# Optimization experiments

Measured on AMD Instinct MI355X. Metric: run time of the kernel, lower is better.

The kernel has to match this reference:

```python
import jax, jax.numpy as jnp
import numpy as np

Bsz, T, N, Dm = 4, 256, 32, 128
L, S, DC = 2, 16, 4          # num_layers, d_state, d_conv
DI = 2 * Dm                   # d_inner (expand=2)
DTR = Dm // 16                # dt_rank = ceil(128/16) = 8
K, R = 4, 16                  # K_bases, rank
MAX_DT = 0.2

def _silu(x):
    return x * jax.nn.sigmoid(x)

def _causal_dwconv(x, w, b):
    # x: [BN, T, DI], w: [DI, DC] depthwise, left-pad DC-1 (== pad DC-1 both sides then [:T])
    xc = jnp.swapaxes(x, 1, 2)  # [BN, DI, T]
    y = jax.lax.conv_general_dilated(xc, w[:, None, :], (1,), [(DC - 1, 0)],
                                     feature_group_count=DI,
                                     dimension_numbers=('NCH', 'OIH', 'NCH'))
    return jnp.swapaxes(y + b[None, :, None], 1, 2)

def _selective_scan(x, dt, Bm, Cm, A):
    # x, dt: [BN,T,DI]; Bm, Cm: [BN,T,S]; A: [DI,S]
    def step(carry, inp):
        dt_t, B_t, C_t, x_t = inp
        dA = jnp.exp(dt_t[:, :, None] * A)                      # [BN,DI,S]
        carry = dA * carry + dt_t[:, :, None] * B_t[:, None, :] * x_t[:, :, None]
        y = jnp.einsum('bds,bs->bd', carry, C_t)
        return carry, y
    BN = x.shape[0]
    carry0 = jnp.zeros((BN, DI, S), x.dtype)
    seq = (jnp.swapaxes(dt, 0, 1), jnp.swapaxes(Bm, 0, 1),
           jnp.swapaxes(Cm, 0, 1), jnp.swapaxes(x, 0, 1))
    _, ys = jax.lax.scan(step, carry0, seq)
    return jnp.swapaxes(ys, 0, 1)

def _mamba(h, in_w, cw, cb, xw, dtw, dtb, A_log, Dp, ow):
    xz = h @ in_w.T                          # [BN,T,2*DI]
    xh, z = xz[..., :DI], xz[..., DI:]
    xh = _silu(_causal_dwconv(xh, cw, cb))
    x_dbl = xh @ xw.T                        # [BN,T,DTR+2S]
    dt = jax.nn.softplus(x_dbl[..., :DTR] @ dtw.T + dtb)
    Bm = x_dbl[..., DTR:DTR + S]
    Cm = x_dbl[..., DTR + S:]
    A = -jnp.exp(A_log)
    y = _selective_scan(xh, dt, Bm, Cm, A) + Dp * xh
    return (y * _silu(z)) @ ow.T

def setup_inputs():
    ks = jax.random.split(jax.random.key(0), 32)
    n = lambda i, shp, s: jax.random.normal(ks[i], shp, jnp.float32) * s
    sD = 1.0 / np.sqrt(Dm); sI = 1.0 / np.sqrt(DI)
    return {
        'x': n(0, (Bsz, T, N, Dm), 1.0),
        'in_proj_w': n(1, (L, 2 * DI, Dm), sD),
        'conv_w': n(2, (L, DI, DC), 1.0 / np.sqrt(DC)),
        'conv_b': n(3, (L, DI), 0.01),
        'x_proj_w': n(4, (L, DTR + 2 * S, DI), sI),
        'dt_proj_w': n(5, (L, DI, DTR), 1.0 / np.sqrt(DTR)),
        'dt_proj_b': jnp.full((L, DI), -4.0, jnp.float32) + n(6, (L, DI), 0.1),
        'A_log': jnp.tile(jnp.log(jnp.arange(1, S + 1, dtype=jnp.float32))[None, None, :], (L, DI, 1)),
        'D_skip': jnp.ones((L, DI), jnp.float32),
        'out_proj_w': n(7, (L, Dm, DI), sI),
        'U': n(8, (K, Dm, R), sD),
        'V': n(9, (K, R, Dm), sD),
        'A_scale': jnp.full((K,), 0.3, jnp.float32),
        'gate_w1': n(10, (Dm, Dm), sD), 'gate_b1': jnp.zeros((Dm,), jnp.float32),
        'gate_w2': n(11, (K + 1, Dm), sD), 'gate_b2': jnp.zeros((K + 1,), jnp.float32),
        'film_g_w': n(12, (Dm, Dm), sD), 'film_g_b': jnp.zeros((Dm,), jnp.float32),
        'film_b_w': n(13, (Dm, Dm), sD), 'film_b_b': jnp.zeros((Dm,), jnp.float32),
        'mix_w1': n(14, (Dm, Dm), sD), 'mix_b1': jnp.zeros((Dm,), jnp.float32),
        'mix_w2': n(15, (1, Dm), sD), 'mix_b2': jnp.zeros((1,), jnp.float32),
    }

def reference(x, in_proj_w, conv_w, conv_b, x_proj_w, dt_proj_w, dt_proj_b, A_log, D_skip, out_proj_w, U, V, A_scale, gate_w1, gate_b1, gate_w2, gate_b2, film_g_w, film_g_b, film_b_w, film_b_b, mix_w1, mix_b1, mix_w2, mix_b2):
    B, T_, N_, D_ = x.shape
    h = x.transpose(0, 2, 1, 3).reshape(B * N_, T_, D_)   # [BN,T,D]
    for l in range(L):  # residual Mamba stack
        h = h + _mamba(h, in_proj_w[l], conv_w[l], conv_b[l], x_proj_w[l],
                       dt_proj_w[l], dt_proj_b[l], A_log[l], D_skip[l], out_proj_w[l])
    gate_out = jax.nn.gelu(h @ gate_w1.T + gate_b1, approximate=False) @ gate_w2.T + gate_b2
    w = jax.nn.softmax(gate_out[..., :K], axis=-1)        # [BN,T,K]
    dt = jax.nn.sigmoid(gate_out[..., K:]) * MAX_DT       # [BN,T,1]
    U_eff = U * A_scale[:, None, None]
    def amix(hh):
        hU = jnp.einsum('btd,kdr->btkr', hh, U_eff)
        hUV = jnp.einsum('btkr,krd->btkd', hU, V)
        return jnp.einsum('btkd,btk->btd', hUV, w)
    hA = amix(h)
    hA2 = amix(hA)  # taylor_order == 2
    upd_nl = jnp.tanh(dt * hA + 0.5 * dt ** 2 * hA2)
    gamma = jnp.tanh(h @ film_g_w.T + film_g_b)
    beta = jnp.tanh(h @ film_b_w.T + film_b_b)
    upd_nl = gamma * upd_nl + beta
    g = jax.nn.sigmoid(jax.nn.gelu(h @ mix_w1.T + mix_b1, approximate=False) @ mix_w2.T + mix_b2)
    h_dyn = h + g * upd_nl
    return h_dyn.reshape(B, N_, T_, D_).transpose(0, 2, 1, 3)
```

## Files before the change

kernel.cpp:

```cpp
#include <hip/hip_runtime.h>
#include <math.h>

#define BSZ   4
#define TT    256
#define NN    32
#define DM    128
#define LL    2
#define SS    16
#define DCV   4
#define DI    256
#define DTR   8
#define KK    4
#define RR    16
#define BN_   128
#define TOK   32768

typedef _Float16 f16x8 __attribute__((ext_vector_type(8)));
typedef float    f32x4 __attribute__((ext_vector_type(4)));

__device__ __forceinline__ float sigm(float x) { return __fdividef(1.f, 1.f + __expf(-x)); }

__global__ __launch_bounds__(256) void pack_h_k(const float* __restrict__ x, float* __restrict__ h)
{
    int tid = threadIdx.x;
    int d = tid & 127;
    int tok = blockIdx.x * 2 + (tid >> 7);
    int t = tok & 255;
    int bn = tok >> 8;
    int b = bn >> 5, n = bn & 31;
    h[(size_t)tok * DM + d] = x[(((size_t)b * TT + t) * NN + n) * DM + d];
}

template<int EPI, int ACT>
__global__ __launch_bounds__(256)
void mgemm_k(const float* __restrict__ A, int lda,
             const float* __restrict__ W,
             const float* __restrict__ bias,
             float* C, int ldc,
             int N, int K,
             const float* __restrict__ aux, int auxb)
{
    __shared__ char smem[24576];

    const int tid  = threadIdx.x;
    const int lane = tid & 63;
    const int wv   = tid >> 6;
    const long row0 = (long)blockIdx.y * 128;
    const int  colb = blockIdx.x * 64;
    const int  NC   = K >> 5;

    const int st_rc = tid >> 2;
    const int st_g  = tid & 3;
    const int offA0 = st_rc * 64        + ((st_g ^ (st_rc & 3)) << 4);
    const int offA1 = (st_rc + 64) * 64 + ((st_g ^ (st_rc & 3)) << 4);
    const int offW  = st_rc * 64        + ((st_g ^ (st_rc & 3)) << 4);
    const int wcol  = colb + st_rc;
    const bool wok  = (wcol < N);

    const int fr = lane & 15;
    const int fg = lane >> 4;
    const int ra0 = (wv << 5) + fr;
    const int offa0 = ra0 * 64        + ((fg ^ (ra0 & 3)) << 4);
    const int offa1 = (ra0 + 16) * 64 + ((fg ^ (ra0 & 3)) << 4);
    int offb[4];
#pragma unroll
    for (int nj = 0; nj < 4; ++nj) {
        int cb = (nj << 4) + fr;
        offb[nj] = cb * 64 + ((fg ^ (fr & 3)) << 4);
    }

    f32x4 acc[2][4];
#pragma unroll
    for (int mi = 0; mi < 2; ++mi)
#pragma unroll
        for (int nj = 0; nj < 4; ++nj) acc[mi][nj] = (f32x4){0.f, 0.f, 0.f, 0.f};

    float va0[8], va1[8], vw[8];

    {
        const float* pa0 = A + (row0 + st_rc) * (long)lda + st_g * 8;
        *(float4*)&va0[0] = *(const float4*)pa0;
        *(float4*)&va0[4] = *(const float4*)(pa0 + 4);
        const float* pa1 = pa0 + 64 * (long)lda;
        *(float4*)&va1[0] = *(const float4*)pa1;
        *(float4*)&va1[4] = *(const float4*)(pa1 + 4);
        if (wok) {
            const float* pw = W + (long)wcol * K + st_g * 8;
            *(float4*)&vw[0] = *(const float4*)pw;
            *(float4*)&vw[4] = *(const float4*)(pw + 4);
        } else {
#pragma unroll
            for (int j = 0; j < 8; ++j) vw[j] = 0.f;
        }
    }
    {
        char* base = smem;
        f16x8 h0, h1, hw;
#pragma unroll
        for (int j = 0; j < 8; ++j) { h0[j] = (_Float16)va0[j]; h1[j] = (_Float16)va1[j]; hw[j] = (_Float16)vw[j]; }
        *(f16x8*)(base + offA0) = h0;
        *(f16x8*)(base + offA1) = h1;
        *(f16x8*)(base + 8192 + offW) = hw;
    }
    __syncthreads();

    for (int c = 0; c < NC; ++c) {
        if (c + 1 < NC) {
            const int kk = (c + 1) << 5;
            const float* pa0 = A + (row0 + st_rc) * (long)lda + kk + st_g * 8;
            *(float4*)&va0[0] = *(const float4*)pa0;
            *(float4*)&va0[4] = *(const float4*)(pa0 + 4);
            const float* pa1 = pa0 + 64 * (long)lda;
            *(float4*)&va1[0] = *(const float4*)pa1;
            *(float4*)&va1[4] = *(const float4*)(pa1 + 4);
            if (wok) {
                const float* pw = W + (long)wcol * K + kk + st_g * 8;
                *(float4*)&vw[0] = *(const float4*)pw;
                *(float4*)&vw[4] = *(const float4*)(pw + 4);
            }
        }
        {
            const char* As = smem + (c & 1) * 12288;
            const char* Ws = As + 8192;
            f16x8 af0 = *(const f16x8*)(As + offa0);
            f16x8 af1 = *(const f16x8*)(As + offa1);
            f16x8 bf[4];
#pragma unroll
            for (int nj = 0; nj < 4; ++nj) bf[nj] = *(const f16x8*)(Ws + offb[nj]);
#pragma unroll
            for (int nj = 0; nj < 4; ++nj) {
                acc[0][nj] = __builtin_amdgcn_mfma_f32_16x16x32_f16(af0, bf[nj], acc[0][nj], 0, 0, 0);
                acc[1][nj] = __builtin_amdgcn_mfma_f32_16x16x32_f16(af1, bf[nj], acc[1][nj], 0, 0, 0);
            }
        }
        if (c + 1 < NC) {
            char* base = smem + ((c + 1) & 1) * 12288;
            f16x8 h0, h1, hw;
#pragma unroll
            for (int j = 0; j < 8; ++j) { h0[j] = (_Float16)va0[j]; h1[j] = (_Float16)va1[j]; hw[j] = (_Float16)vw[j]; }
            *(f16x8*)(base + offA0) = h0;
            *(f16x8*)(base + offA1) = h1;
            *(f16x8*)(base + 8192 + offW) = hw;
        }
        __syncthreads();
    }

#pragma unroll
    for (int nj = 0; nj < 4; ++nj) {
        int col = colb + (nj << 4) + fr;
        if (col < N) {
            float bb = 0.f;
            if (EPI == 1 && bias) bb = bias[col];
#pragma unroll
            for (int mi = 0; mi < 2; ++mi) {
                long rg = row0 + (wv << 5) + (mi << 4) + (fg << 2);
#pragma unroll
                for (int r = 0; r < 4; ++r) {
                    float v = acc[mi][nj][r];
                    if (EPI == 1) {
                        v += bb;
                        if (ACT == 1) v = 0.5f * v * (1.f + erff(v * 0.70710678118654752f));
                        else if (ACT == 2) v = tanhf(v);
                    } else if (EPI == 6) {
                        v *= aux[(rg + r) * 4 + ((col >> 4) + auxb)];
                    }
                    float* pc = C + (rg + r) * (long)ldc + col;
                    if (EPI == 4) *pc += v;
                    else          *pc = v;
                }
            }
        }
    }
}

template<int BM, int BN, int TM, int TN, int EPI>
__global__ __launch_bounds__(256)
void gemm_k(const float* __restrict__ A, int lda,
            const float* __restrict__ W,
            const float* __restrict__ bias,
            float* C, int ldc,
            int M, int N, int K,
            const float* __restrict__ aux)
{
    constexpr int BK = 16;
    constexpr int LDS_A = BM + 4;
    constexpr int LDS_B = BN + 4;
    static_assert((BM / TM) * (BN / TN) == 256, "256 threads");
    constexpr int NA = BM * BK / 1024;
    constexpr int NB = BN * BK / 1024;

    __shared__ float As[BK][LDS_A];
    __shared__ float Ws[BK][LDS_B];

    const int tid = threadIdx.x;
    constexpr int nx = BN / TN;
    const int tx = tid % nx, ty = tid / nx;
    const long row0 = (long)blockIdx.y * BM;
    const long col0 = (long)blockIdx.x * BN;

    float acc[TM][TN];
#pragma unroll
    for (int i = 0; i < TM; i++)
#pragma unroll
        for (int j = 0; j < TN; j++) acc[i][j] = 0.f;

    for (int kk = 0; kk < K; kk += BK) {
        float4 a_reg[NA], w_reg[NB];
#pragma unroll
        for (int i = 0; i < NA; ++i) {
            int idx = i * 1024 + tid * 4;
            int r = idx >> 4, k0 = idx & 15;
            int k = kk + k0;
            const float* p = A + (row0 + r) * (long)lda + k;
            a_reg[i] = *(const float4*)p;
        }
#pragma unroll
        for (int i = 0; i < NB; ++i) {
            int idx = i * 1024 + tid * 4;
            int r = idx >> 4, k0 = idx & 15;
            long gc = col0 + r;
            int k = kk + k0;
            if (gc < N) {
                const float* p = W + gc * (long)K + k;
                w_reg[i] = *(const float4*)p;
            } else w_reg[i] = make_float4(0.f, 0.f, 0.f, 0.f);
        }
        __syncthreads();
#pragma unroll
        for (int i = 0; i < NA; ++i) {
            int idx = i * 1024 + tid * 4;
            int r = idx >> 4, k0 = idx & 15;
            As[k0 + 0][r] = a_reg[i].x; As[k0 + 1][r] = a_reg[i].y;
            As[k0 + 2][r] = a_reg[i].z; As[k0 + 3][r] = a_reg[i].w;
        }
#pragma unroll
        for (int i = 0; i < NB; ++i) {
            int idx = i * 1024 + tid * 4;
            int r = idx >> 4, k0 = idx & 15;
            Ws[k0 + 0][r] = w_reg[i].x; Ws[k0 + 1][r] = w_reg[i].y;
            Ws[k0 + 2][r] = w_reg[i].z; Ws[k0 + 3][r] = w_reg[i].w;
        }
        __syncthreads();
#pragma unroll
        for (int k = 0; k < BK; ++k) {
            float a_f[TM], w_f[TN];
#pragma unroll
            for (int i = 0; i < TM; i += 4)
                *(float4*)&a_f[i] = *(const float4*)&As[k][ty * TM + i];
#pragma unroll
            for (int j = 0; j < TN; j += 4)
                *(float4*)&w_f[j] = *(const float4*)&Ws[k][tx * TN + j];
#pragma unroll
            for (int i = 0; i < TM; i++)
#pragma unroll
                for (int j = 0; j < TN; j++)
                    acc[i][j] = fmaf(a_f[i], w_f[j], acc[i][j]);
        }
    }
#pragma unroll
    for (int i = 0; i < TM; i++) {
        long r = row0 + ty * TM + i;
#pragma unroll
        for (int j = 0; j < TN; j++) {
            long c = col0 + tx * TN + j;
            if (c < N) C[r * ldc + c] = acc[i][j];
        }
    }
}

__global__ __launch_bounds__(256) void conv_silu_k(const float* __restrict__ xz,
                                                   const float* __restrict__ cw,
                                                   const float* __restrict__ cb,
                                                   float* __restrict__ xh)
{
    int c = threadIdx.x;
    int t0 = blockIdx.x << 2;
    int bn = blockIdx.y;
    float w0 = cw[c * 4 + 0], w1 = cw[c * 4 + 1], w2 = cw[c * 4 + 2], w3 = cw[c * 4 + 3];
    float bb = cb[c];
    size_t base = ((size_t)bn * TT + t0) * 512 + c;
    float xm3 = (t0 >= 3) ? xz[base - 1536] : 0.f;
    float xm2 = (t0 >= 2) ? xz[base - 1024] : 0.f;
    float xm1 = (t0 >= 1) ? xz[base - 512]  : 0.f;
    float x0 = xz[base];
    float x1 = xz[base + 512];
    float x2 = xz[base + 1024];
    float x3 = xz[base + 1536];
    float o0 = bb + w3 * x0 + w2 * xm1 + w1 * xm2 + w0 * xm3;
    float o1 = bb + w3 * x1 + w2 * x0  + w1 * xm1 + w0 * xm2;
    float o2 = bb + w3 * x2 + w2 * x1  + w1 * x0  + w0 * xm1;
    float o3 = bb + w3 * x3 + w2 * x2  + w1 * x1  + w0 * x0;
    size_t ob = ((size_t)bn * TT + t0) * DI + c;
    xh[ob]           = o0 * sigm(o0);
    xh[ob + DI]      = o1 * sigm(o1);
    xh[ob + 2 * DI]  = o2 * sigm(o2);
    xh[ob + 3 * DI]  = o3 * sigm(o3);
}

__global__ __launch_bounds__(256) void dt_k(const float* __restrict__ xdbl,
                                            const float* __restrict__ dtw,
                                            const float* __restrict__ dtb,
                                            float* __restrict__ dtout)
{
    int n = threadIdx.x;
    int tok = blockIdx.x;
    const float* xr = xdbl + (size_t)tok * 40;
    float acc = dtb[n];
#pragma unroll
    for (int k = 0; k < 8; k++) acc = fmaf(xr[k], dtw[n * 8 + k], acc);
    float sp = fmaxf(acc, 0.f) + __logf(1.f + __expf(-fabsf(acc)));
    dtout[(size_t)tok * 512 + n] = sp;
}

#define SCH 16
__global__ __launch_bounds__(256) void scan_k(const float* __restrict__ xz,
                                              const float* xhp,
                                              const float* __restrict__ xdbl,
                                              const float* __restrict__ A_log,
                                              const float* __restrict__ Dp,
                                              float* yg)
{
    __shared__ float sdt[2][SCH][128];
    __shared__ float sxv[2][SCH][128];
    __shared__ float szz[2][SCH][128];
    __shared__ float sbc[2][SCH][32];

    const int tid  = threadIdx.x;
    const int lane = tid & 63;
    const int wave = tid >> 6;
    const int sh   = lane >> 5;
    const int dloc = (wave << 5) + (lane & 31);
    const int bn   = blockIdx.y;
    const int dbase= blockIdx.x << 7;
    const int d    = dbase + dloc;
    const size_t tokb = (size_t)bn * TT;

    float A[8];
#pragma unroll
    for (int q = 0; q < 8; ++q)
        A[q] = -__expf(A_log[d * SS + sh * 8 + q]);
    const float Dv = Dp[d];

    float st[8];
#pragma unroll
    for (int q = 0; q < 8; ++q) st[q] = 0.f;

    const int st0 = tid >> 5,        sc0 = (tid & 31) << 2;
    const int st1 = (tid + 256) >> 5, sc1 = (tid & 31) << 2;
    const int bstep = tid >> 3, bq = (tid & 7) << 2;
    float4 rdt[2], rxv[2], rz[2], rbc;

#define STAGE_ISSUE(TB) do {                                              \
    size_t tb_ = tokb + (TB);                                             \
    rdt[0] = *(const float4*)&xz [(tb_ + st0) * 512 + dbase + sc0];       \
    rdt[1] = *(const float4*)&xz [(tb_ + st1) * 512 + dbase + sc1];       \
    rxv[0] = *(const float4*)&xhp[(tb_ + st0) * DI  + dbase + sc0];       \
    rxv[1] = *(const float4*)&xhp[(tb_ + st1) * DI  + dbase + sc1];       \
    rz [0] = *(const float4*)&xz [(tb_ + st0) * 512 + 256 + dbase + sc0]; \
    rz [1] = *(const float4*)&xz [(tb_ + st1) * 512 + 256 + dbase + sc1]; \
    if (tid < 128) rbc = *(const float4*)&xdbl[(tb_ + bstep) * 40 + 8 + bq]; \
} while (0)

#define STAGE_WRITE(B) do {                                               \
    *(float4*)&sdt[B][st0][sc0] = rdt[0];                                 \
    *(float4*)&sdt[B][st1][sc1] = rdt[1];                                 \
    *(float4*)&sxv[B][st0][sc0] = rxv[0];                                 \
    *(float4*)&sxv[B][st1][sc1] = rxv[1];                                 \
    *(float4*)&szz[B][st0][sc0] = rz[0];                                  \
    *(float4*)&szz[B][st1][sc1] = rz[1];                                  \
    if (tid < 128) *(float4*)&sbc[B][bstep][bq] = rbc;                    \
} while (0)

    STAGE_ISSUE(0);
    STAGE_WRITE(0);
    __syncthreads();

    for (int c = 0; c < TT / SCH; ++c) {
        const int b = c & 1;
        if (c + 1 < TT / SCH) STAGE_ISSUE((c + 1) * SCH);
        const int tb = c * SCH;
#pragma unroll
        for (int s = 0; s < SCH; ++s) {
            float dt_c = sdt[b][s][dloc];
            float xv_c = sxv[b][s][dloc];
            float z_c  = szz[b][s][dloc];
            float4 B0c = *(const float4*)&sbc[b][s][sh * 8];
            float4 B1c = *(const float4*)&sbc[b][s][sh * 8 + 4];
            float4 C0c = *(const float4*)&sbc[b][s][16 + sh * 8];
            float4 C1c = *(const float4*)&sbc[b][s][16 + sh * 8 + 4];

            float dtx = dt_c * xv_c;
            float dA0 = __expf(A[0] * dt_c);
            float dA1 = __expf(A[1] * dt_c);
            float dA2 = __expf(A[2] * dt_c);
            float dA3 = __expf(A[3] * dt_c);
            float dA4 = __expf(A[4] * dt_c);
            float dA5 = __expf(A[5] * dt_c);
            float dA6 = __expf(A[6] * dt_c);
            float dA7 = __expf(A[7] * dt_c);
            st[0] = fmaf(dA0, st[0], dtx * B0c.x);
            st[1] = fmaf(dA1, st[1], dtx * B0c.y);
            st[2] = fmaf(dA2, st[2], dtx * B0c.z);
            st[3] = fmaf(dA3, st[3], dtx * B0c.w);
            st[4] = fmaf(dA4, st[4], dtx * B1c.x);
            st[5] = fmaf(dA5, st[5], dtx * B1c.y);
            st[6] = fmaf(dA6, st[6], dtx * B1c.z);
            st[7] = fmaf(dA7, st[7], dtx * B1c.w);
            float y0 = st[0] * C0c.x;
            float y1 = st[1] * C0c.y;
            y0 = fmaf(st[2], C0c.z, y0);
            y1 = fmaf(st[3], C0c.w, y1);
            y0 = fmaf(st[4], C1c.x, y0);
            y1 = fmaf(st[5], C1c.y, y1);
            y0 = fmaf(st[6], C1c.z, y0);
            y1 = fmaf(st[7], C1c.w, y1);
            float y = y0 + y1;
            y += __shfl_xor(y, 32, 64);
            float zg = __fdividef(z_c, 1.f + __expf(-z_c));
            float outv = (y + Dv * xv_c) * zg;
            if (sh == 0) yg[(tokb + tb + s) * DI + d] = outv;
        }
        if (c + 1 < TT / SCH) STAGE_WRITE(b ^ 1);
        __syncthreads();
    }
#undef STAGE_ISSUE
#undef STAGE_WRITE
}

__global__ __launch_bounds__(256) void gate_k(const float* __restrict__ gmb,
                                              const float* __restrict__ gw2,
                                              const float* __restrict__ gb2,
                                              const float* __restrict__ mw2,
                                              const float* __restrict__ mb2,
                                              const float* __restrict__ Ascale,
                                              float* __restrict__ ws4,
                                              float* __restrict__ dts,
                                              float* __restrict__ gs)
{
    int l = threadIdx.x & 63;
    int tok = blockIdx.x * 4 + (threadIdx.x >> 6);
    const float* g1 = gmb + (size_t)tok * 512;
    float a0 = g1[l], a1 = g1[l + 64];
    float m0 = g1[128 + l], m1v = g1[192 + l];
    float p[5];
#pragma unroll
    for (int j = 0; j < 5; j++)
        p[j] = a0 * gw2[j * DM + l] + a1 * gw2[j * DM + l + 64];
    float q = m0 * mw2[l] + m1v * mw2[l + 64];
#pragma unroll
    for (int off = 32; off; off >>= 1) {
#pragma unroll
        for (int j = 0; j < 5; j++) p[j] += __shfl_xor(p[j], off, 64);
        q += __shfl_xor(q, off, 64);
    }
    if (l == 0) {
        float go[5];
#pragma unroll
        for (int j = 0; j < 5; j++) go[j] = p[j] + gb2[j];
        float mx = fmaxf(fmaxf(go[0], go[1]), fmaxf(go[2], go[3]));
        float e[4], sum = 0.f;
#pragma unroll
        for (int k = 0; k < 4; k++) { e[k] = expf(go[k] - mx); sum += e[k]; }
        float inv = 1.f / sum;
#pragma unroll
        for (int k = 0; k < 4; k++) ws4[(size_t)tok * 4 + k] = e[k] * inv * Ascale[k];
        dts[tok] = 0.2f * sigm(go[4]);
        gs[tok]  = sigm(q + mb2[0]);
    }
}

__global__ __launch_bounds__(256) void pack_uv_k(const float* __restrict__ U,
                                                 const float* __restrict__ V,
                                                 float* __restrict__ Wu,
                                                 float* __restrict__ Wv)
{
    int i = blockIdx.x * 256 + threadIdx.x;
    if (i < 8192) {
        int kr = i >> 7, d = i & 127;
        int k = kr >> 4, r = kr & 15;
        Wu[i] = U[((size_t)k * DM + d) * RR + r];
        int d2 = i >> 6, kr2 = i & 63;
        int k2 = kr2 >> 4, r2 = kr2 & 15;
        Wv[i] = V[((size_t)k2 * RR + r2) * DM + d2];
    }
}

__global__ __launch_bounds__(256) void pack_cat_k(const float* __restrict__ gw1,
                                                  const float* __restrict__ gb1,
                                                  const float* __restrict__ mw1,
                                                  const float* __restrict__ mb1,
                                                  const float* __restrict__ fgw,
                                                  const float* __restrict__ fgb,
                                                  const float* __restrict__ fbw,
                                                  const float* __restrict__ fbb,
                                                  float* __restrict__ Wcat,
                                                  float* __restrict__ bcat)
{
    int i = blockIdx.x * 256 + threadIdx.x;
    if (i < 65536) {
        int r = i >> 7, k = i & 127;
        int sel = r >> 7;
        int rr = r & 127;
        const float* src = (sel == 0) ? gw1 : (sel == 1) ? mw1 : (sel == 2) ? fgw : fbw;
        Wcat[i] = src[rr * DM + k];
    }
    if (i < 512) {
        int sel = i >> 7, rr = i & 127;
        const float* src = (sel == 0) ? gb1 : (sel == 1) ? mb1 : (sel == 2) ? fgb : fbb;
        bcat[i] = src[rr];
    }
}

__global__ __launch_bounds__(256) void combine_k(const float* __restrict__ h,
                                                 const float* __restrict__ hA,
                                                 const float* __restrict__ hA2,
                                                 const float* __restrict__ gmb,
                                                 const float* __restrict__ dts,
                                                 const float* __restrict__ gs,
                                                 float* __restrict__ out)
{
    int tid = threadIdx.x;
    int d = tid & 127;
    int tok = blockIdx.x * 2 + (tid >> 7);
    int t = tok & 255;
    int bn = tok >> 8;
    int b = bn >> 5, n = bn & 31;
    float dtv = dts[tok], gv = gs[tok];
    size_t i = (size_t)tok * DM + d;
    float u = tanhf(dtv * hA[i] + 0.5f * dtv * dtv * hA2[i]);
    float gamma = gmb[(size_t)tok * 512 + 256 + d];
    float beta  = gmb[(size_t)tok * 512 + 384 + d];
    u = gamma * u + beta;
    out[(((size_t)b * TT + t) * NN + n) * DM + d] = h[i] + gv * u;
}

extern "C" void kernel_launch(void* const* d_in, const int* in_sizes, int n_in,
                              void* d_out, int out_size, void* d_ws, size_t ws_size,
                              hipStream_t stream)
{
    const float* x       = (const float*)d_in[0];
    const float* in_w    = (const float*)d_in[1];
    const float* conv_w  = (const float*)d_in[2];
    const float* conv_b  = (const float*)d_in[3];
    const float* xpw     = (const float*)d_in[4];
    const float* dtw     = (const float*)d_in[5];
    const float* dtb     = (const float*)d_in[6];
    const float* A_log   = (const float*)d_in[7];
    const float* D_skip  = (const float*)d_in[8];
    const float* ow      = (const float*)d_in[9];
    const float* U       = (const float*)d_in[10];
    const float* V       = (const float*)d_in[11];
    const float* Ascale  = (const float*)d_in[12];
    const float* gw1     = (const float*)d_in[13];
    const float* gb1     = (const float*)d_in[14];
    const float* gw2     = (const float*)d_in[15];
    const float* gb2     = (const float*)d_in[16];
    const float* fgw     = (const float*)d_in[17];
    const float* fgb     = (const float*)d_in[18];
    const float* fbw     = (const float*)d_in[19];
    const float* fbb     = (const float*)d_in[20];
    const float* mw1     = (const float*)d_in[21];
    const float* mb1     = (const float*)d_in[22];
    const float* mw2     = (const float*)d_in[23];
    const float* mb2     = (const float*)d_in[24];

    float* ws = (float*)d_ws;
    float* h    = ws;
    float* xz   = h + 4194304;
    float* xh   = xz + 16777216;
    float* xdbl = xh + 8388608;

    pack_h_k<<<TOK / 2, 256, 0, stream>>>(x, h);

    for (int l = 0; l < LL; ++l) {
        const float* iw = in_w + (size_t)l * 512 * 128;
        mgemm_k<0,0><<<dim3(8,256), 256, 0, stream>>>(
            h, DM, iw, nullptr, xz, 512, 512, 128, nullptr, 0);
        conv_silu_k<<<dim3(TT / 4, BN_), 256, 0, stream>>>(
            xz, conv_w + (size_t)l * DI * DCV, conv_b + (size_t)l * DI, xh);
        gemm_k<64,64,4,4,0><<<dim3(1,512), 256, 0, stream>>>(
            xh, DI, xpw + (size_t)l * 40 * DI, nullptr, xdbl, 40, TOK, 40, DI, nullptr);
        dt_k<<<TOK, 256, 0, stream>>>(
            xdbl, dtw + (size_t)l * DI * DTR, dtb + (size_t)l * DI, xz);
        scan_k<<<dim3(2, BN_), 256, 0, stream>>>(
            xz, xh, xdbl, A_log + (size_t)l * DI * SS, D_skip + (size_t)l * DI, xh);
        mgemm_k<4,0><<<dim3(2,256), 256, 0, stream>>>(
            xh, DI, ow + (size_t)l * DM * DI, nullptr, h, DM, 128, 256, nullptr, 0);
    }

    float* gmb  = xz;
    float* Zb   = xz;
    float* hA   = xh;
    float* hA2  = xh + 4194304;
    float* Wcat = xdbl;
    float* bcat = xdbl + 65536;
    float* Wu   = xdbl + 66048;
    float* Wv   = xdbl + 74240;
    float* ws4  = xdbl + 82432;
    float* dts  = xdbl + 213504;
    float* gs   = xdbl + 246272;

    pack_cat_k<<<256, 256, 0, stream>>>(gw1, gb1, mw1, mb1, fgw, fgb, fbw, fbb, Wcat, bcat);
    mgemm_k<1,1><<<dim3(4,256), 256, 0, stream>>>(
        h, DM, Wcat, bcat, gmb, 512, 256, 128, nullptr, 0);
    mgemm_k<1,2><<<dim3(4,256), 256, 0, stream>>>(
        h, DM, Wcat + 256 * 128, bcat + 256, gmb + 256, 512, 256, 128, nullptr, 0);
    gate_k<<<TOK / 4, 256, 0, stream>>>(gmb, gw2, gb2, mw2, mb2, Ascale, ws4, dts, gs);
    pack_uv_k<<<32, 256, 0, stream>>>(U, V, Wu, Wv);

    mgemm_k<6,0><<<dim3(1,256), 256, 0, stream>>>(
        h, DM, Wu, nullptr, Zb, 512, 64, 128, ws4, 0);
    mgemm_k<0,0><<<dim3(2,256), 256, 0, stream>>>(
        Zb, 512, Wv, nullptr, hA, DM, 128, 64, nullptr, 0);
    mgemm_k<6,0><<<dim3(1,256), 256, 0, stream>>>(
        hA, DM, Wu, nullptr, Zb, 512, 64, 128, ws4, 0);
    mgemm_k<0,0><<<dim3(2,256), 256, 0, stream>>>(
        Zb, 512, Wv, nullptr, hA2, DM, 128, 64, nullptr, 0);

    combine_k<<<TOK / 2, 256, 0, stream>>>(h, hA, hA2, gmb, dts, gs, (float*)d_out);
}
```

Baseline: 584.2 us.

## Fuse dt projection and softplus into scan kernel and split state across more threads

Removes the separate dt_k kernel. The scan kernel now computes dt from the staged x_dbl rows in shared memory, so the full-size dt tensor is never written to or read back from global memory. The scan block grows to 512 threads, each holding 4 state elements instead of 8, which adds one more cross-lane shuffle reduction. This gives each block more parallel lanes but adds an extra __syncthreads per chunk plus the dt compute on the critical path.

```diff
diff --git a/kernel.cpp b/kernel.cpp
--- a/kernel.cpp
+++ b/kernel.cpp
@@ -297,25 +297,12 @@
     xh[ob + 3 * DI]  = o3 * sigm(o3);
 }
 
-__global__ __launch_bounds__(256) void dt_k(const float* __restrict__ xdbl,
-                                            const float* __restrict__ dtw,
-                                            const float* __restrict__ dtb,
-                                            float* __restrict__ dtout)
-{
-    int n = threadIdx.x;
-    int tok = blockIdx.x;
-    const float* xr = xdbl + (size_t)tok * 40;
-    float acc = dtb[n];
-#pragma unroll
-    for (int k = 0; k < 8; k++) acc = fmaf(xr[k], dtw[n * 8 + k], acc);
-    float sp = fmaxf(acc, 0.f) + __logf(1.f + __expf(-fabsf(acc)));
-    dtout[(size_t)tok * 512 + n] = sp;
-}
-
 #define SCH 16
-__global__ __launch_bounds__(256) void scan_k(const float* __restrict__ xz,
+__global__ __launch_bounds__(512) void scan_k(const float* __restrict__ xz,
                                               const float* xhp,
                                               const float* __restrict__ xdbl,
+                                              const float* __restrict__ dtw,
+                                              const float* __restrict__ dtb,
                                               const float* __restrict__ A_log,
                                               const float* __restrict__ Dp,
                                               float* yg)
@@ -324,107 +311,122 @@
     __shared__ float sxv[2][SCH][128];
     __shared__ float szz[2][SCH][128];
     __shared__ float sbc[2][SCH][32];
+    __shared__ float sxd[2][SCH][8];
 
     const int tid  = threadIdx.x;
     const int lane = tid & 63;
     const int wave = tid >> 6;
-    const int sh   = lane >> 5;
-    const int dloc = (wave << 5) + (lane & 31);
+    const int sq   = lane >> 4;
+    const int dloc = (wave << 4) + (lane & 15);
     const int bn   = blockIdx.y;
     const int dbase= blockIdx.x << 7;
     const int d    = dbase + dloc;
     const size_t tokb = (size_t)bn * TT;
 
-    float A[8];
-#pragma unroll
-    for (int q = 0; q < 8; ++q)
-        A[q] = -__expf(A_log[d * SS + sh * 8 + q]);
+    float A[4];
+#pragma unroll
+    for (int q = 0; q < 4; ++q)
+        A[q] = -__expf(A_log[d * SS + sq * 4 + q]);
     const float Dv = Dp[d];
 
-    float st[8];
-#pragma unroll
-    for (int q = 0; q < 8; ++q) st[q] = 0.f;
-
-    const int st0 = tid >> 5,        sc0 = (tid & 31) << 2;
-    const int st1 = (tid + 256) >> 5, sc1 = (tid & 31) << 2;
+    float st[4];
+#pragma unroll
+    for (int q = 0; q < 4; ++q) st[q] = 0.f;
+
+    const int st0 = tid >> 5;
+    const int sc0 = (tid & 31) << 2;
     const int bstep = tid >> 3, bq = (tid & 7) << 2;
-    float4 rdt[2], rxv[2], rz[2], rbc;
+    const int xi = tid - 128;
+    const int xr = xi >> 1, xc4 = (xi & 1) << 2;
+    float4 rxv, rzz, rbc, rxd;
+
+    const int dt_s  = tid >> 5;
+    const int dt_d4 = (tid & 31) << 2;
+    float dtwv[4][8];
+    float dtbv[4];
+#pragma unroll
+    for (int j = 0; j < 4; ++j) {
+        const float* p = dtw + (size_t)(dbase + dt_d4 + j) * 8;
+        *(float4*)&dtwv[j][0] = *(const float4*)p;
+        *(float4*)&dtwv[j][4] = *(const float4*)(p + 4);
+        dtbv[j] = dtb[dbase + dt_d4 + j];
+    }
 
 #define STAGE_ISSUE(TB) do {                                              \
     size_t tb_ = tokb + (TB);                                             \
-    rdt[0] = *(const float4*)&xz [(tb_ + st0) * 512 + dbase + sc0];       \
-    rdt[1] = *(const float4*)&xz [(tb_ + st1) * 512 + dbase + sc1];       \
-    rxv[0] = *(const float4*)&xhp[(tb_ + st0) * DI  + dbase + sc0];       \
-    rxv[1] = *(const float4*)&xhp[(tb_ + st1) * DI  + dbase + sc1];       \
-    rz [0] = *(const float4*)&xz [(tb_ + st0) * 512 + 256 + dbase + sc0]; \
-    rz [1] = *(const float4*)&xz [(tb_ + st1) * 512 + 256 + dbase + sc1]; \
+    rxv = *(const float4*)&xhp[(tb_ + st0) * DI + dbase + sc0];           \
+    rzz = *(const float4*)&xz [(tb_ + st0) * 512 + 256 + dbase + sc0];    \
     if (tid < 128) rbc = *(const float4*)&xdbl[(tb_ + bstep) * 40 + 8 + bq]; \
+    else if (tid < 160) rxd = *(const float4*)&xdbl[(tb_ + xr) * 40 + xc4]; \
 } while (0)
 
 #define STAGE_WRITE(B) do {                                               \
-    *(float4*)&sdt[B][st0][sc0] = rdt[0];                                 \
-    *(float4*)&sdt[B][st1][sc1] = rdt[1];                                 \
-    *(float4*)&sxv[B][st0][sc0] = rxv[0];                                 \
-    *(float4*)&sxv[B][st1][sc1] = rxv[1];                                 \
-    *(float4*)&szz[B][st0][sc0] = rz[0];                                  \
-    *(float4*)&szz[B][st1][sc1] = rz[1];                                  \
+    *(float4*)&sxv[B][st0][sc0] = rxv;                                    \
+    *(float4*)&szz[B][st0][sc0] = rzz;                                    \
     if (tid < 128) *(float4*)&sbc[B][bstep][bq] = rbc;                    \
+    else if (tid < 160) *(float4*)&sxd[B][xr][xc4] = rxd;                 \
+} while (0)
+
+#define DT_COMPUTE(B) do {                                                \
+    float4 o_;                                                            \
+    _Pragma("unroll")                                                     \
+    for (int j = 0; j < 4; ++j) {                                         \
+        float v_ = dtbv[j];                                               \
+        _Pragma("unroll")                                                 \
+        for (int k = 0; k < 8; ++k)                                       \
+            v_ = fmaf(sxd[B][dt_s][k], dtwv[j][k], v_);                   \
+        o_[j] = fmaxf(v_, 0.f) + __logf(1.f + __expf(-fabsf(v_)));        \
+    }                                                                     \
+    *(float4*)&sdt[B][dt_s][dt_d4] = o_;                                  \
 } while (0)
 
     STAGE_ISSUE(0);
     STAGE_WRITE(0);
     __syncthreads();
+    DT_COMPUTE(0);
+    __syncthreads();
 
     for (int c = 0; c < TT / SCH; ++c) {
         const int b = c & 1;
-        if (c + 1 < TT / SCH) STAGE_ISSUE((c + 1) * SCH);
+        const bool more = (c + 1 < TT / SCH);
+        if (more) STAGE_ISSUE((c + 1) * SCH);
         const int tb = c * SCH;
 #pragma unroll
         for (int s = 0; s < SCH; ++s) {
             float dt_c = sdt[b][s][dloc];
             float xv_c = sxv[b][s][dloc];
             float z_c  = szz[b][s][dloc];
-            float4 B0c = *(const float4*)&sbc[b][s][sh * 8];
-            float4 B1c = *(const float4*)&sbc[b][s][sh * 8 + 4];
-            float4 C0c = *(const float4*)&sbc[b][s][16 + sh * 8];
-            float4 C1c = *(const float4*)&sbc[b][s][16 + sh * 8 + 4];
+            float4 B4 = *(const float4*)&sbc[b][s][sq << 2];
+            float4 C4 = *(const float4*)&sbc[b][s][16 + (sq << 2)];
 
             float dtx = dt_c * xv_c;
             float dA0 = __expf(A[0] * dt_c);
             float dA1 = __expf(A[1] * dt_c);
             float dA2 = __expf(A[2] * dt_c);
             float dA3 = __expf(A[3] * dt_c);
-            float dA4 = __expf(A[4] * dt_c);
-            float dA5 = __expf(A[5] * dt_c);
-            float dA6 = __expf(A[6] * dt_c);
-            float dA7 = __expf(A[7] * dt_c);
-            st[0] = fmaf(dA0, st[0], dtx * B0c.x);
-            st[1] = fmaf(dA1, st[1], dtx * B0c.y);
-            st[2] = fmaf(dA2, st[2], dtx * B0c.z);
-            st[3] = fmaf(dA3, st[3], dtx * B0c.w);
-            st[4] = fmaf(dA4, st[4], dtx * B1c.x);
-            st[5] = fmaf(dA5, st[5], dtx * B1c.y);
-            st[6] = fmaf(dA6, st[6], dtx * B1c.z);
-            st[7] = fmaf(dA7, st[7], dtx * B1c.w);
-            float y0 = st[0] * C0c.x;
-            float y1 = st[1] * C0c.y;
-            y0 = fmaf(st[2], C0c.z, y0);
-            y1 = fmaf(st[3], C0c.w, y1);
-            y0 = fmaf(st[4], C1c.x, y0);
-            y1 = fmaf(st[5], C1c.y, y1);
-            y0 = fmaf(st[6], C1c.z, y0);
-            y1 = fmaf(st[7], C1c.w, y1);
+            st[0] = fmaf(dA0, st[0], dtx * B4.x);
+            st[1] = fmaf(dA1, st[1], dtx * B4.y);
+            st[2] = fmaf(dA2, st[2], dtx * B4.z);
+            st[3] = fmaf(dA3, st[3], dtx * B4.w);
+            float y0 = st[0] * C4.x;
+            float y1 = st[1] * C4.y;
+            y0 = fmaf(st[2], C4.z, y0);
+            y1 = fmaf(st[3], C4.w, y1);
             float y = y0 + y1;
+            y += __shfl_xor(y, 16, 64);
             y += __shfl_xor(y, 32, 64);
             float zg = __fdividef(z_c, 1.f + __expf(-z_c));
             float outv = (y + Dv * xv_c) * zg;
-            if (sh == 0) yg[(tokb + tb + s) * DI + d] = outv;
-        }
-        if (c + 1 < TT / SCH) STAGE_WRITE(b ^ 1);
+            if (sq == 0) yg[(tokb + tb + s) * DI + d] = outv;
+        }
+        if (more) STAGE_WRITE(b ^ 1);
+        __syncthreads();
+        if (more) DT_COMPUTE(b ^ 1);
         __syncthreads();
     }
 #undef STAGE_ISSUE
 #undef STAGE_WRITE
+#undef DT_COMPUTE
 }
 
 __global__ __launch_bounds__(256) void gate_k(const float* __restrict__ gmb,
@@ -580,10 +582,9 @@
             xz, conv_w + (size_t)l * DI * DCV, conv_b + (size_t)l * DI, xh);
         gemm_k<64,64,4,4,0><<<dim3(1,512), 256, 0, stream>>>(
             xh, DI, xpw + (size_t)l * 40 * DI, nullptr, xdbl, 40, TOK, 40, DI, nullptr);
-        dt_k<<<TOK, 256, 0, stream>>>(
-            xdbl, dtw + (size_t)l * DI * DTR, dtb + (size_t)l * DI, xz);
-        scan_k<<<dim3(2, BN_), 256, 0, stream>>>(
-            xz, xh, xdbl, A_log + (size_t)l * DI * SS, D_skip + (size_t)l * DI, xh);
+        scan_k<<<dim3(2, BN_), 512, 0, stream>>>(
+            xz, xh, xdbl, dtw + (size_t)l * DI * DTR, dtb + (size_t)l * DI,
+            A_log + (size_t)l * DI * SS, D_skip + (size_t)l * DI, xh);
         mgemm_k<4,0><<<dim3(2,256), 256, 0, stream>>>(
             xh, DI, ow + (size_t)l * DM * DI, nullptr, h, DM, 128, 256, nullptr, 0);
     }
```

New measurement: 543.9 us. 1.07x faster.
